# Kernel optimization log

Hardware: AMD Instinct MI355X
Metric: run time of the kernel (lower is better)

## Reference

```python
import jax, jax.numpy as jnp
import numpy as np

N_NODES = 100000
N_EDGES = 625000
D_IN = 128
D_OUT = 128


def setup_inputs() -> dict:
    key = jax.random.key(0)
    k1, k2, k3, k4, k5 = jax.random.split(key, 5)
    feature = jax.random.normal(k1, (N_NODES, D_IN), dtype=jnp.float32)
    W = jax.random.normal(k2, (D_OUT, D_IN), dtype=jnp.float32) * (1.0 / np.sqrt(D_IN))
    b = jax.random.normal(k3, (D_OUT,), dtype=jnp.float32) * 0.01
    src = jax.random.randint(k4, (N_EDGES,), 0, N_NODES, dtype=jnp.int64)
    dst = jax.random.randint(k5, (N_EDGES,), 0, N_NODES, dtype=jnp.int64)
    return {"feature": feature, "W": W, "b": b, "src": src, "dst": dst}


def reference(feature, W, b, src, dst):
    # copy_src: gather source-node features along edges -> [E, D_IN]
    msg = feature[src]
    # mean reduce over incoming edges per destination node
    agg = jax.ops.segment_sum(msg, dst, num_segments=N_NODES)  # [N, D_IN]
    deg = jax.ops.segment_sum(jnp.ones((dst.shape[0],), feature.dtype), dst,
                              num_segments=N_NODES)  # [N]
    # DGL mean leaves nodes with zero in-degree at 0
    h = jnp.where(deg[:, None] > 0, agg / jnp.maximum(deg, 1.0)[:, None], 0.0)
    # nn.Linear: h @ W.T + b
    return h @ W.T + b
```

## Files before the change

kernel.cpp:

```cpp
#include <hip/hip_runtime.h>

#define D 128
#define CAP 32

typedef __attribute__((ext_vector_type(8))) short short8;
typedef __attribute__((ext_vector_type(4))) float f32x4;

__device__ __forceinline__ unsigned short f2bf_rne(float x) {
    unsigned int u = __float_as_uint(x);
    u += 0x7fffu + ((u >> 16) & 1u);
    return (unsigned short)(u >> 16);
}

__device__ __forceinline__ unsigned int pack_bf2(float x, float y) {
    return ((unsigned int)f2bf_rne(y) << 16) | (unsigned int)f2bf_rne(x);
}

__global__ __launch_bounds__(256)
void pack_build(const float* __restrict__ feat, const float* __restrict__ W,
                ushort* __restrict__ fb, ushort* __restrict__ Wb,
                const int* __restrict__ src, const int* __restrict__ dst,
                int* __restrict__ cnt, int* __restrict__ bucket,
                int n4, int n_edges, int edgeBlocks) {
    int bx = blockIdx.x;
    if (bx < edgeBlocks) {
        int e = bx * 256 + threadIdx.x;
        if (e < n_edges) {
            int d = dst[e];
            int p = atomicAdd(cnt + d, 1);
            if (p < CAP) bucket[(size_t)d * CAP + p] = src[e];
        }
        return;
    }
    int i = (bx - edgeBlocks) * 256 + threadIdx.x;
    if (i < n4) {
        float4 v = ((const float4*)feat)[i];
        ushort4 o;
        o.x = f2bf_rne(v.x); o.y = f2bf_rne(v.y);
        o.z = f2bf_rne(v.z); o.w = f2bf_rne(v.w);
        ((ushort4*)fb)[i] = o;
    } else if (i < n4 + 32) {
        ((ushort4*)fb)[i] = make_ushort4(0, 0, 0, 0);
    } else if (i < n4 + 32 + 4096) {
        int j = i - (n4 + 32);
        float4 v = ((const float4*)W)[j];
        ushort4 o;
        o.x = f2bf_rne(v.x); o.y = f2bf_rne(v.y);
        o.z = f2bf_rne(v.z); o.w = f2bf_rne(v.w);
        ((ushort4*)Wb)[j] = o;
    }
}

__global__ __launch_bounds__(256)
void agg_gemm(const ushort* __restrict__ fb,
              const int* __restrict__ cnt,
              const int* __restrict__ bucket,
              const ushort* __restrict__ Wb,
              const float* __restrict__ b,
              float* __restrict__ out,
              int n_nodes) {
    __shared__ ushort hs[32 * 136];
    int t = threadIdx.x;
    int lane = t & 63;
    int wave = t >> 6;
    int nb = blockIdx.x * 32;
    int base = nb + wave * 8;

    int hi = lane >> 5;
    int l31 = lane & 31;
    int half32 = lane & 32;

    int myc = (lane < 8) ? cnt[base + lane] : 0;

    unsigned int so = ((unsigned int)hi << 7) + (unsigned int)l31;
    const int* bkt = bucket + (size_t)base * CAP;
    int ids0 = bkt[ 0 + so];
    int ids1 = bkt[32 + so];
    int ids2 = bkt[64 + so];
    int ids3 = bkt[96 + so];

    int d0 = __shfl(myc, 0), d1 = __shfl(myc, 1), d2 = __shfl(myc, 2), d3 = __shfl(myc, 3);
    int d4 = __shfl(myc, 4), d5 = __shfl(myc, 5), d6 = __shfl(myc, 6), d7 = __shfl(myc, 7);
    int c0 = min(d0, CAP), c1 = min(d1, CAP), c2 = min(d2, CAP), c3 = min(d3, CAP);
    int c4 = min(d4, CAP), c5 = min(d5, CAP), c6 = min(d6, CAP), c7 = min(d7, CAP);

    int ms0 = hi ? c4 : c0;
    int ms1 = hi ? c5 : c1;
    int ms2 = hi ? c6 : c2;
    int ms3 = hi ? c7 : c3;
    ids0 = (l31 < ms0) ? ids0 : n_nodes;
    ids1 = (l31 < ms1) ? ids1 : n_nodes;
    ids2 = (l31 < ms2) ? ids2 : n_nodes;
    ids3 = (l31 < ms3) ? ids3 : n_nodes;

    int mm01 = c0 > c1 ? c0 : c1;
    int mm23 = c2 > c3 ? c2 : c3;
    int mm45 = c4 > c5 ? c4 : c5;
    int mm67 = c6 > c7 ? c6 : c7;
    int mmA = mm01 > mm23 ? mm01 : mm23;
    int mmB = mm45 > mm67 ? mm45 : mm67;
    int mmax = mmA > mmB ? mmA : mmB;

    float a00=0,a01=0,a02=0,a03=0;
    float a10=0,a11=0,a12=0,a13=0;
    float a20=0,a21=0,a22=0,a23=0;
    float a30=0,a31=0,a32=0,a33=0;

    const char* fbb = (const char*)fb;
    unsigned int colb = (unsigned int)l31 * 8u;

    for (int j = 0; j < mmax; j += 4) {
        uint2 v0[4], v1[4], v2[4], v3[4];
#pragma unroll
        for (int i = 0; i < 4; ++i) {
            int sl = half32 + j + i;
            unsigned int r0 = (unsigned int)__shfl(ids0, sl);
            unsigned int r1 = (unsigned int)__shfl(ids1, sl);
            unsigned int r2 = (unsigned int)__shfl(ids2, sl);
            unsigned int r3 = (unsigned int)__shfl(ids3, sl);
            v0[i] = *(const uint2*)(fbb + ((r0 << 8) + colb));
            v1[i] = *(const uint2*)(fbb + ((r1 << 8) + colb));
            v2[i] = *(const uint2*)(fbb + ((r2 << 8) + colb));
            v3[i] = *(const uint2*)(fbb + ((r3 << 8) + colb));
        }
#pragma unroll
        for (int i = 0; i < 4; ++i) {
            a00 += __uint_as_float(v0[i].x << 16); a01 += __uint_as_float(v0[i].x & 0xffff0000u);
            a02 += __uint_as_float(v0[i].y << 16); a03 += __uint_as_float(v0[i].y & 0xffff0000u);
            a10 += __uint_as_float(v1[i].x << 16); a11 += __uint_as_float(v1[i].x & 0xffff0000u);
            a12 += __uint_as_float(v1[i].y << 16); a13 += __uint_as_float(v1[i].y & 0xffff0000u);
            a20 += __uint_as_float(v2[i].x << 16); a21 += __uint_as_float(v2[i].x & 0xffff0000u);
            a22 += __uint_as_float(v2[i].y << 16); a23 += __uint_as_float(v2[i].y & 0xffff0000u);
            a30 += __uint_as_float(v3[i].x << 16); a31 += __uint_as_float(v3[i].x & 0xffff0000u);
            a32 += __uint_as_float(v3[i].y << 16); a33 += __uint_as_float(v3[i].y & 0xffff0000u);
        }
    }

    float invc = (myc > 0) ? 1.0f / (float)myc : 0.0f;
    int selidx = half32 >> 3;
    float inv0 = __shfl(invc, 0 + selidx);
    float inv1 = __shfl(invc, 1 + selidx);
    float inv2 = __shfl(invc, 2 + selidx);
    float inv3 = __shfl(invc, 3 + selidx);

    unsigned int* hsu = (unsigned int*)hs;
    int r0 = wave * 8 + hi * 4;
    int cu = l31 * 2;
    *(uint2*)&hsu[(r0 + 0) * 68 + cu] = make_uint2(pack_bf2(a00*inv0, a01*inv0), pack_bf2(a02*inv0, a03*inv0));
    *(uint2*)&hsu[(r0 + 1) * 68 + cu] = make_uint2(pack_bf2(a10*inv1, a11*inv1), pack_bf2(a12*inv1, a13*inv1));
    *(uint2*)&hsu[(r0 + 2) * 68 + cu] = make_uint2(pack_bf2(a20*inv2, a21*inv2), pack_bf2(a22*inv2, a23*inv2));
    *(uint2*)&hsu[(r0 + 3) * 68 + cu] = make_uint2(pack_bf2(a30*inv3, a31*inv3), pack_bf2(a32*inv3, a33*inv3));
    __syncthreads();

    int mt = wave & 1;
    int nh = wave >> 1;
    int lane16 = lane & 15;
    int lq = lane >> 4;

    f32x4 acc[4] = {{0,0,0,0},{0,0,0,0},{0,0,0,0},{0,0,0,0}};
#pragma unroll
    for (int ks = 0; ks < 4; ++ks) {
        short8 afrg = *(const short8*)&hs[(mt * 16 + lane16) * 136 + ks * 32 + lq * 8];
#pragma unroll
        for (int tt = 0; tt < 4; ++tt) {
            short8 bfrg = *(const short8*)&Wb[(size_t)(nh * 64 + tt * 16 + lane16) * D + ks * 32 + lq * 8];
            acc[tt] = __builtin_amdgcn_mfma_f32_16x16x32_bf16(afrg, bfrg, acc[tt], 0, 0, 0);
        }
    }

#pragma unroll
    for (int tt = 0; tt < 4; ++tt) {
        int o = nh * 64 + tt * 16 + lane16;
        float bb = b[o];
        int node = nb + mt * 16 + lq * 4;
#pragma unroll
        for (int r = 0; r < 4; ++r) {
            out[(size_t)(node + r) * D + o] = acc[tt][r] + bb;
        }
    }
}

extern "C" void kernel_launch(void* const* d_in, const int* in_sizes, int n_in,
                              void* d_out, int out_size, void* d_ws, size_t ws_size,
                              hipStream_t stream) {
    const float* feat = (const float*)d_in[0];
    const float* W    = (const float*)d_in[1];
    const float* bia  = (const float*)d_in[2];
    const int* src = (const int*)d_in[3];
    const int* dst = (const int*)d_in[4];
    float* out = (float*)d_out;

    int n_nodes = in_sizes[0] / D;
    int n_edges = in_sizes[3];

    size_t off = 0;
    auto alloc = [&](size_t bytes) { size_t p = off; off = (off + bytes + 4095) & ~(size_t)4095; return p; };
    size_t cnt_off    = alloc((size_t)n_nodes * sizeof(int));
    size_t bucket_off = alloc((size_t)n_nodes * CAP * sizeof(int));
    size_t wb_off     = alloc((size_t)D * D * sizeof(ushort));
    size_t fb_off     = alloc((size_t)(n_nodes + 1) * D * sizeof(ushort));

    int*    cnt    = (int*)((char*)d_ws + cnt_off);
    int*    bucket = (int*)((char*)d_ws + bucket_off);
    ushort* Wb     = (ushort*)((char*)d_ws + wb_off);
    ushort* fb     = (ushort*)((char*)d_ws + fb_off);

    int n4 = n_nodes * (D / 4);
    int G  = n4 + 32 + (D * D / 4);

    int edgeBlocks = (n_edges + 255) / 256;
    int packBlocks = (G + 255) / 256;

    hipMemsetAsync(cnt, 0, (size_t)n_nodes * sizeof(int), stream);
    pack_build<<<edgeBlocks + packBlocks, 256, 0, stream>>>(feat, W, fb, Wb, src, dst,
                                                            cnt, bucket, n4, n_edges, edgeBlocks);
    agg_gemm<<<n_nodes / 32, 256, 0, stream>>>(fb, cnt, bucket, Wb, bia, out, n_nodes);
}
```

Measured before the change: 185.8 us.

## Remap gather to 16-lane groups with 16B loads and software-pipelined prefetch

The aggregation loop is restructured so each 16-lane group handles one destination row with 16-byte loads, so each wave covers two rows per group instead of four rows per half-wave with 8-byte loads. A software pipeline issues the gathers for edges j+2..j+5 before accumulating the earlier ones, hiding gather latency. Launch bounds now request 4 blocks per SM to steer register allocation. The mmax reduction uses xor shuffles, and out-of-range edges read a zero padding row. The cost is more live registers from the prefetched uint4 buffers.

```diff
diff --git a/kernel.cpp b/kernel.cpp
--- a/kernel.cpp
+++ b/kernel.cpp
@@ -51,7 +51,7 @@
     }
 }
 
-__global__ __launch_bounds__(256)
+__global__ __launch_bounds__(256, 4)
 void agg_gemm(const ushort* __restrict__ fb,
               const int* __restrict__ cnt,
               const int* __restrict__ bucket,
@@ -66,90 +66,78 @@
     int nb = blockIdx.x * 32;
     int base = nb + wave * 8;
 
-    int hi = lane >> 5;
-    int l31 = lane & 31;
-    int half32 = lane & 32;
+    int g = lane >> 4;
+    int s = lane & 15;
+    int g16 = lane & 48;
 
     int myc = (lane < 8) ? cnt[base + lane] : 0;
 
-    unsigned int so = ((unsigned int)hi << 7) + (unsigned int)l31;
     const int* bkt = bucket + (size_t)base * CAP;
-    int ids0 = bkt[ 0 + so];
-    int ids1 = bkt[32 + so];
-    int ids2 = bkt[64 + so];
-    int ids3 = bkt[96 + so];
-
-    int d0 = __shfl(myc, 0), d1 = __shfl(myc, 1), d2 = __shfl(myc, 2), d3 = __shfl(myc, 3);
-    int d4 = __shfl(myc, 4), d5 = __shfl(myc, 5), d6 = __shfl(myc, 6), d7 = __shfl(myc, 7);
-    int c0 = min(d0, CAP), c1 = min(d1, CAP), c2 = min(d2, CAP), c3 = min(d3, CAP);
-    int c4 = min(d4, CAP), c5 = min(d5, CAP), c6 = min(d6, CAP), c7 = min(d7, CAP);
-
-    int ms0 = hi ? c4 : c0;
-    int ms1 = hi ? c5 : c1;
-    int ms2 = hi ? c6 : c2;
-    int ms3 = hi ? c7 : c3;
-    ids0 = (l31 < ms0) ? ids0 : n_nodes;
-    ids1 = (l31 < ms1) ? ids1 : n_nodes;
-    ids2 = (l31 < ms2) ? ids2 : n_nodes;
-    ids3 = (l31 < ms3) ? ids3 : n_nodes;
-
-    int mm01 = c0 > c1 ? c0 : c1;
-    int mm23 = c2 > c3 ? c2 : c3;
-    int mm45 = c4 > c5 ? c4 : c5;
-    int mm67 = c6 > c7 ? c6 : c7;
-    int mmA = mm01 > mm23 ? mm01 : mm23;
-    int mmB = mm45 > mm67 ? mm45 : mm67;
-    int mmax = mmA > mmB ? mmA : mmB;
-
-    float a00=0,a01=0,a02=0,a03=0;
-    float a10=0,a11=0,a12=0,a13=0;
-    float a20=0,a21=0,a22=0,a23=0;
-    float a30=0,a31=0,a32=0,a33=0;
+    int idsA0 = bkt[g * 32 + s];
+    int idsA1 = bkt[g * 32 + 16 + s];
+    int idsB0 = bkt[128 + g * 32 + s];
+    int idsB1 = bkt[128 + g * 32 + 16 + s];
+
+    int dA = __shfl(myc, g);
+    int dB = __shfl(myc, 4 + g);
+    int cA = min(dA, CAP), cB = min(dB, CAP);
+    idsA0 = (s < cA)      ? idsA0 : n_nodes;
+    idsA1 = (16 + s < cA) ? idsA1 : n_nodes;
+    idsB0 = (s < cB)      ? idsB0 : n_nodes;
+    idsB1 = (16 + s < cB) ? idsB1 : n_nodes;
+
+    int mm = cA > cB ? cA : cB;
+    mm = max(mm, __shfl_xor(mm, 16));
+    mm = max(mm, __shfl_xor(mm, 32));
+    int mmax = mm;
+
+    float fA[8], fB[8];
+#pragma unroll
+    for (int i = 0; i < 8; ++i) { fA[i] = 0.0f; fB[i] = 0.0f; }
 
     const char* fbb = (const char*)fb;
-    unsigned int colb = (unsigned int)l31 * 8u;
-
+    unsigned int colb = (unsigned int)s * 16u;
+
+#define GATH1(dst, ids0_, ids1_, jj) { \
+    int idr_ = ((jj) < 16) ? (ids0_) : (ids1_); \
+    unsigned int rr_ = ((jj) < mmax) ? (unsigned int)__shfl(idr_, g16 + ((jj) & 15)) \
+                                     : (unsigned int)n_nodes; \
+    dst = *(const uint4*)(fbb + ((rr_ << 8) + colb)); }
+
+#define ACC8(v, f) { \
+    f[0] += __uint_as_float((v).x << 16); f[1] += __uint_as_float((v).x & 0xffff0000u); \
+    f[2] += __uint_as_float((v).y << 16); f[3] += __uint_as_float((v).y & 0xffff0000u); \
+    f[4] += __uint_as_float((v).z << 16); f[5] += __uint_as_float((v).z & 0xffff0000u); \
+    f[6] += __uint_as_float((v).w << 16); f[7] += __uint_as_float((v).w & 0xffff0000u); }
+
+    uint4 a0, b0, a1, b1, a2, b2, a3, b3;
+    GATH1(a0, idsA0, idsA1, 0); GATH1(b0, idsB0, idsB1, 0);
+    GATH1(a1, idsA0, idsA1, 1); GATH1(b1, idsB0, idsB1, 1);
     for (int j = 0; j < mmax; j += 4) {
-        uint2 v0[4], v1[4], v2[4], v3[4];
-#pragma unroll
-        for (int i = 0; i < 4; ++i) {
-            int sl = half32 + j + i;
-            unsigned int r0 = (unsigned int)__shfl(ids0, sl);
-            unsigned int r1 = (unsigned int)__shfl(ids1, sl);
-            unsigned int r2 = (unsigned int)__shfl(ids2, sl);
-            unsigned int r3 = (unsigned int)__shfl(ids3, sl);
-            v0[i] = *(const uint2*)(fbb + ((r0 << 8) + colb));
-            v1[i] = *(const uint2*)(fbb + ((r1 << 8) + colb));
-            v2[i] = *(const uint2*)(fbb + ((r2 << 8) + colb));
-            v3[i] = *(const uint2*)(fbb + ((r3 << 8) + colb));
-        }
-#pragma unroll
-        for (int i = 0; i < 4; ++i) {
-            a00 += __uint_as_float(v0[i].x << 16); a01 += __uint_as_float(v0[i].x & 0xffff0000u);
-            a02 += __uint_as_float(v0[i].y << 16); a03 += __uint_as_float(v0[i].y & 0xffff0000u);
-            a10 += __uint_as_float(v1[i].x << 16); a11 += __uint_as_float(v1[i].x & 0xffff0000u);
-            a12 += __uint_as_float(v1[i].y << 16); a13 += __uint_as_float(v1[i].y & 0xffff0000u);
-            a20 += __uint_as_float(v2[i].x << 16); a21 += __uint_as_float(v2[i].x & 0xffff0000u);
-            a22 += __uint_as_float(v2[i].y << 16); a23 += __uint_as_float(v2[i].y & 0xffff0000u);
-            a30 += __uint_as_float(v3[i].x << 16); a31 += __uint_as_float(v3[i].x & 0xffff0000u);
-            a32 += __uint_as_float(v3[i].y << 16); a33 += __uint_as_float(v3[i].y & 0xffff0000u);
-        }
-    }
-
-    float invc = (myc > 0) ? 1.0f / (float)myc : 0.0f;
-    int selidx = half32 >> 3;
-    float inv0 = __shfl(invc, 0 + selidx);
-    float inv1 = __shfl(invc, 1 + selidx);
-    float inv2 = __shfl(invc, 2 + selidx);
-    float inv3 = __shfl(invc, 3 + selidx);
+        GATH1(a2, idsA0, idsA1, j + 2); GATH1(b2, idsB0, idsB1, j + 2);
+        GATH1(a3, idsA0, idsA1, j + 3); GATH1(b3, idsB0, idsB1, j + 3);
+        ACC8(a0, fA); ACC8(b0, fB);
+        ACC8(a1, fA); ACC8(b1, fB);
+        GATH1(a0, idsA0, idsA1, j + 4); GATH1(b0, idsB0, idsB1, j + 4);
+        GATH1(a1, idsA0, idsA1, j + 5); GATH1(b1, idsB0, idsB1, j + 5);
+        ACC8(a2, fA); ACC8(b2, fB);
+        ACC8(a3, fA); ACC8(b3, fB);
+    }
+#undef GATH1
+#undef ACC8
+
+    float invA = dA > 0 ? 1.0f / (float)dA : 0.0f;
+    float invB = dB > 0 ? 1.0f / (float)dB : 0.0f;
 
     unsigned int* hsu = (unsigned int*)hs;
-    int r0 = wave * 8 + hi * 4;
-    int cu = l31 * 2;
-    *(uint2*)&hsu[(r0 + 0) * 68 + cu] = make_uint2(pack_bf2(a00*inv0, a01*inv0), pack_bf2(a02*inv0, a03*inv0));
-    *(uint2*)&hsu[(r0 + 1) * 68 + cu] = make_uint2(pack_bf2(a10*inv1, a11*inv1), pack_bf2(a12*inv1, a13*inv1));
-    *(uint2*)&hsu[(r0 + 2) * 68 + cu] = make_uint2(pack_bf2(a20*inv2, a21*inv2), pack_bf2(a22*inv2, a23*inv2));
-    *(uint2*)&hsu[(r0 + 3) * 68 + cu] = make_uint2(pack_bf2(a30*inv3, a31*inv3), pack_bf2(a32*inv3, a33*inv3));
+    int rA = wave * 8 + g;
+    int rB = wave * 8 + 4 + g;
+    *(uint4*)&hsu[rA * 68 + s * 4] = make_uint4(
+        pack_bf2(fA[0] * invA, fA[1] * invA), pack_bf2(fA[2] * invA, fA[3] * invA),
+        pack_bf2(fA[4] * invA, fA[5] * invA), pack_bf2(fA[6] * invA, fA[7] * invA));
+    *(uint4*)&hsu[rB * 68 + s * 4] = make_uint4(
+        pack_bf2(fB[0] * invB, fB[1] * invB), pack_bf2(fB[2] * invB, fB[3] * invB),
+        pack_bf2(fB[4] * invB, fB[5] * invB), pack_bf2(fB[6] * invB, fB[7] * invB));
     __syncthreads();
 
     int mt = wave & 1;
```

New measurement: 180.2 us. 3.0% less time.

## Apply linear transform before aggregation and fuse GEMM into packing kernel

Applied to the files above, without the earlier changes.

Moves the feature transform ahead of the mean aggregation using linearity. The pre kernel now computes bf16 X·W^T per node with MFMA, staging W in LDS. The aggregation kernel then gathers transformed rows, scales by the inverse degree and adds the bias, with no shared-memory staging or barrier. This removes the separate bf16 pack pass and the in-kernel GEMM after aggregation. In exchange, W is converted to bf16 redundantly in every GEMM block and each of those blocks uses 32 KB of LDS.

```diff
diff --git a/kernel.cpp b/kernel.cpp
--- a/kernel.cpp
+++ b/kernel.cpp
@@ -17,14 +17,16 @@
 }
 
 __global__ __launch_bounds__(256)
-void pack_build(const float* __restrict__ feat, const float* __restrict__ W,
-                ushort* __restrict__ fb, ushort* __restrict__ Wb,
-                const int* __restrict__ src, const int* __restrict__ dst,
-                int* __restrict__ cnt, int* __restrict__ bucket,
-                int n4, int n_edges, int edgeBlocks) {
+void pre(const float* __restrict__ feat, const float* __restrict__ W,
+         ushort* __restrict__ xw,
+         const int* __restrict__ src, const int* __restrict__ dst,
+         int* __restrict__ cnt, int* __restrict__ bucket,
+         int n_nodes, int n_edges, int edgeBlocks) {
+    __shared__ ushort wlds[D * D];
     int bx = blockIdx.x;
+    int t = threadIdx.x;
     if (bx < edgeBlocks) {
-        int e = bx * 256 + threadIdx.x;
+        int e = bx * 256 + t;
         if (e < n_edges) {
             int d = dst[e];
             int p = atomicAdd(cnt + d, 1);
@@ -32,34 +34,63 @@
         }
         return;
     }
-    int i = (bx - edgeBlocks) * 256 + threadIdx.x;
-    if (i < n4) {
-        float4 v = ((const float4*)feat)[i];
+    if (bx == edgeBlocks) {
+        if (t < 16) ((uint4*)(xw + (size_t)n_nodes * D))[t] = make_uint4(0, 0, 0, 0);
+        return;
+    }
+    for (int i = t; i < D * D / 4; i += 256) {
+        float4 v = ((const float4*)W)[i];
         ushort4 o;
         o.x = f2bf_rne(v.x); o.y = f2bf_rne(v.y);
         o.z = f2bf_rne(v.z); o.w = f2bf_rne(v.w);
-        ((ushort4*)fb)[i] = o;
-    } else if (i < n4 + 32) {
-        ((ushort4*)fb)[i] = make_ushort4(0, 0, 0, 0);
-    } else if (i < n4 + 32 + 4096) {
-        int j = i - (n4 + 32);
-        float4 v = ((const float4*)W)[j];
-        ushort4 o;
-        o.x = f2bf_rne(v.x); o.y = f2bf_rne(v.y);
-        o.z = f2bf_rne(v.z); o.w = f2bf_rne(v.w);
-        ((ushort4*)Wb)[j] = o;
-    }
-}
-
-__global__ __launch_bounds__(256)
-void agg_gemm(const ushort* __restrict__ fb,
-              const int* __restrict__ cnt,
-              const int* __restrict__ bucket,
-              const ushort* __restrict__ Wb,
-              const float* __restrict__ b,
-              float* __restrict__ out,
-              int n_nodes) {
-    __shared__ ushort hs[32 * 136];
+        ((ushort4*)wlds)[i] = o;
+    }
+    __syncthreads();
+
+    int lane = t & 63;
+    int wave = t >> 6;
+    int lane16 = lane & 15;
+    int lq = lane >> 4;
+    int gRow = (bx - edgeBlocks - 1) * 64 + wave * 16;
+
+    int arow = gRow + lane16;
+    int arowc = arow < n_nodes ? arow : 0;
+    const float* ap0 = feat + (size_t)arowc * D + lq * 8;
+
+    f32x4 acc[8] = {{0,0,0,0},{0,0,0,0},{0,0,0,0},{0,0,0,0},
+                    {0,0,0,0},{0,0,0,0},{0,0,0,0},{0,0,0,0}};
+#pragma unroll
+    for (int ks = 0; ks < 4; ++ks) {
+        float4 a0 = *(const float4*)(ap0 + ks * 32);
+        float4 a1 = *(const float4*)(ap0 + ks * 32 + 4);
+        union { short8 s; uint4 u; } af;
+        af.u.x = pack_bf2(a0.x, a0.y); af.u.y = pack_bf2(a0.z, a0.w);
+        af.u.z = pack_bf2(a1.x, a1.y); af.u.w = pack_bf2(a1.z, a1.w);
+#pragma unroll
+        for (int tt = 0; tt < 8; ++tt) {
+            short8 bfrg = *(const short8*)&wlds[(tt * 16 + lane16) * D + ks * 32 + lq * 8];
+            acc[tt] = __builtin_amdgcn_mfma_f32_16x16x32_bf16(af.s, bfrg, acc[tt], 0, 0, 0);
+        }
+    }
+#pragma unroll
+    for (int tt = 0; tt < 8; ++tt) {
+        int o = tt * 16 + lane16;
+        int row = gRow + lq * 4;
+#pragma unroll
+        for (int r = 0; r < 4; ++r) {
+            if (row + r < n_nodes)
+                xw[(size_t)(row + r) * D + o] = f2bf_rne(acc[tt][r]);
+        }
+    }
+}
+
+__global__ __launch_bounds__(256, 8)
+void agg(const ushort* __restrict__ xw,
+         const int* __restrict__ cnt,
+         const int* __restrict__ bucket,
+         const float* __restrict__ b,
+         float* __restrict__ out,
+         int n_nodes) {
     int t = threadIdx.x;
     int lane = t & 63;
     int wave = t >> 6;
@@ -106,7 +137,7 @@
     float a20=0,a21=0,a22=0,a23=0;
     float a30=0,a31=0,a32=0,a33=0;
 
-    const char* fbb = (const char*)fb;
+    const char* fbb = (const char*)xw;
     unsigned int colb = (unsigned int)l31 * 8u;
 
     for (int j = 0; j < mmax; j += 4) {
@@ -143,41 +174,18 @@
     float inv2 = __shfl(invc, 2 + selidx);
     float inv3 = __shfl(invc, 3 + selidx);
 
-    unsigned int* hsu = (unsigned int*)hs;
-    int r0 = wave * 8 + hi * 4;
-    int cu = l31 * 2;
-    *(uint2*)&hsu[(r0 + 0) * 68 + cu] = make_uint2(pack_bf2(a00*inv0, a01*inv0), pack_bf2(a02*inv0, a03*inv0));
-    *(uint2*)&hsu[(r0 + 1) * 68 + cu] = make_uint2(pack_bf2(a10*inv1, a11*inv1), pack_bf2(a12*inv1, a13*inv1));
-    *(uint2*)&hsu[(r0 + 2) * 68 + cu] = make_uint2(pack_bf2(a20*inv2, a21*inv2), pack_bf2(a22*inv2, a23*inv2));
-    *(uint2*)&hsu[(r0 + 3) * 68 + cu] = make_uint2(pack_bf2(a30*inv3, a31*inv3), pack_bf2(a32*inv3, a33*inv3));
-    __syncthreads();
-
-    int mt = wave & 1;
-    int nh = wave >> 1;
-    int lane16 = lane & 15;
-    int lq = lane >> 4;
-
-    f32x4 acc[4] = {{0,0,0,0},{0,0,0,0},{0,0,0,0},{0,0,0,0}};
-#pragma unroll
-    for (int ks = 0; ks < 4; ++ks) {
-        short8 afrg = *(const short8*)&hs[(mt * 16 + lane16) * 136 + ks * 32 + lq * 8];
-#pragma unroll
-        for (int tt = 0; tt < 4; ++tt) {
-            short8 bfrg = *(const short8*)&Wb[(size_t)(nh * 64 + tt * 16 + lane16) * D + ks * 32 + lq * 8];
-            acc[tt] = __builtin_amdgcn_mfma_f32_16x16x32_bf16(afrg, bfrg, acc[tt], 0, 0, 0);
-        }
-    }
-
-#pragma unroll
-    for (int tt = 0; tt < 4; ++tt) {
-        int o = nh * 64 + tt * 16 + lane16;
-        float bb = b[o];
-        int node = nb + mt * 16 + lq * 4;
-#pragma unroll
-        for (int r = 0; r < 4; ++r) {
-            out[(size_t)(node + r) * D + o] = acc[tt][r] + bb;
-        }
-    }
+    float4 bb = ((const float4*)b)[l31];
+    int nodeb = base + hi * 4;
+
+    float4 o0 = make_float4(a00*inv0 + bb.x, a01*inv0 + bb.y, a02*inv0 + bb.z, a03*inv0 + bb.w);
+    float4 o1 = make_float4(a10*inv1 + bb.x, a11*inv1 + bb.y, a12*inv1 + bb.z, a13*inv1 + bb.w);
+    float4 o2 = make_float4(a20*inv2 + bb.x, a21*inv2 + bb.y, a22*inv2 + bb.z, a23*inv2 + bb.w);
+    float4 o3 = make_float4(a30*inv3 + bb.x, a31*inv3 + bb.y, a32*inv3 + bb.z, a33*inv3 + bb.w);
+
+    ((float4*)(out + (size_t)(nodeb + 0) * D))[l31] = o0;
+    ((float4*)(out + (size_t)(nodeb + 1) * D))[l31] = o1;
+    ((float4*)(out + (size_t)(nodeb + 2) * D))[l31] = o2;
+    ((float4*)(out + (size_t)(nodeb + 3) * D))[l31] = o3;
 }
 
 extern "C" void kernel_launch(void* const* d_in, const int* in_sizes, int n_in,
@@ -197,22 +205,17 @@
     auto alloc = [&](size_t bytes) { size_t p = off; off = (off + bytes + 4095) & ~(size_t)4095; return p; };
     size_t cnt_off    = alloc((size_t)n_nodes * sizeof(int));
     size_t bucket_off = alloc((size_t)n_nodes * CAP * sizeof(int));
-    size_t wb_off     = alloc((size_t)D * D * sizeof(ushort));
-    size_t fb_off     = alloc((size_t)(n_nodes + 1) * D * sizeof(ushort));
+    size_t xw_off     = alloc((size_t)(n_nodes + 1) * D * sizeof(ushort));
 
     int*    cnt    = (int*)((char*)d_ws + cnt_off);
     int*    bucket = (int*)((char*)d_ws + bucket_off);
-    ushort* Wb     = (ushort*)((char*)d_ws + wb_off);
-    ushort* fb     = (ushort*)((char*)d_ws + fb_off);
-
-    int n4 = n_nodes * (D / 4);
-    int G  = n4 + 32 + (D * D / 4);
+    ushort* xw     = (ushort*)((char*)d_ws + xw_off);
 
     int edgeBlocks = (n_edges + 255) / 256;
-    int packBlocks = (G + 255) / 256;
+    int gemmBlocks = (n_nodes + 63) / 64;
 
     hipMemsetAsync(cnt, 0, (size_t)n_nodes * sizeof(int), stream);
-    pack_build<<<edgeBlocks + packBlocks, 256, 0, stream>>>(feat, W, fb, Wb, src, dst,
-                                                            cnt, bucket, n4, n_edges, edgeBlocks);
-    agg_gemm<<<n_nodes / 32, 256, 0, stream>>>(fb, cnt, bucket, Wb, bia, out, n_nodes);
-}
+    pre<<<edgeBlocks + 1 + gemmBlocks, 256, 0, stream>>>(feat, W, xw, src, dst,
+                                                         cnt, bucket, n_nodes, n_edges, edgeBlocks);
+    agg<<<n_nodes / 32, 256, 0, stream>>>(xw, cnt, bucket, bia, out, n_nodes);
+}
```

Result: slower. 240.6 us (+29.5%).
